# Kernel optimization log

Hardware: AMD Instinct MI355X
Metric: run time of the kernel (lower is better)

## Reference

```python
import jax, jax.numpy as jnp
import numpy as np

B, D, H, O, E = 16384, 256, 256, 256, 32
N_ACTIVE = 22          # int(32 * 0.7) from BoltzmannGate
TEMP = float(np.e)     # Boltzmann temperature
EPS = 1e-8


def setup_inputs() -> dict:
    key = jax.random.key(0)
    ks = jax.random.split(key, 7)
    s = 0.02  # init scale for weights
    return {
        "x":  jax.random.normal(ks[0], (B, D), dtype=jnp.float32),
        "W1": jax.random.normal(ks[1], (E, H, D), dtype=jnp.float32) * s,  # [E, out=H, in=D] torch Linear layout
        "b1": jax.random.normal(ks[2], (E, H), dtype=jnp.float32) * s,
        "W2": jax.random.normal(ks[3], (E, O, H), dtype=jnp.float32) * s,
        "b2": jax.random.normal(ks[4], (E, O), dtype=jnp.float32) * s,
        "Wg": jax.random.normal(ks[5], (E, D), dtype=jnp.float32) * s,
        "bg": jax.random.normal(ks[6], (E,), dtype=jnp.float32) * s,
    }


def reference(x, W1, b1, W2, b2, Wg, bg):
    # Dense all-experts forward: [B, E, H] -> relu -> [B, E, O]
    h = jax.nn.relu(jnp.einsum('bd,ehd->beh', x, W1) + b1[None, :, :])
    expert_out = jnp.einsum('beh,eoh->beo', h, W2) + b2[None, :, :]

    # Boltzmann gate: softmax(scores / T), keep top-k probs, renormalize.
    scores = (x @ Wg.T + bg) / TEMP                      # [B, E]
    probs = jax.nn.softmax(scores, axis=-1)
    _, topk_idx = jax.lax.top_k(probs, N_ACTIVE)         # [B, N_ACTIVE]
    mask = jnp.zeros_like(probs).at[jnp.arange(B)[:, None], topk_idx].set(1.0)
    weights = probs * mask
    weights = weights / (jnp.sum(weights, axis=-1, keepdims=True) + EPS)

    # Weighted combine over experts: [B, O]
    return jnp.einsum('be,beo->bo', weights, expert_out)
```

## Files before the change

kernel.cpp:

```cpp
#include <hip/hip_runtime.h>
#include <hip/hip_bf16.h>


typedef __attribute__((ext_vector_type(8))) short bf16x8;
typedef __attribute__((ext_vector_type(4))) float f32x4;

__device__ __forceinline__ unsigned short f2bf(float f) {
    unsigned u = __builtin_bit_cast(unsigned, f);
    u += 0x7FFFu + ((u >> 16) & 1u);
    return (unsigned short)(u >> 16);
}
__device__ __forceinline__ unsigned pack_bf16x2(float a, float b) {
    return (unsigned)f2bf(a) | ((unsigned)f2bf(b) << 16);
}

#define LX(r, ch) (((r) << 8) + ((((ch) ^ ((r) & 7))) << 3))

__global__ __launch_bounds__(256) void cvt_w(const float* __restrict__ W1,
                                             const float* __restrict__ W2,
                                             unsigned short* __restrict__ Wr) {
    int T = blockIdx.x * 256 + threadIdx.x;
    int lane = T & 63, t = (T >> 6) & 3, kb = (T >> 8) & 7;
    int g = (T >> 11) & 7, e = T >> 14;
    int l15 = lane & 15, quad = lane >> 4;
    int row = (g & 3) * 64 + t * 16 + l15;
    const float* src = ((g < 4) ? W1 : W2) +
                       ((long)e * 256 + row) * 256 + kb * 32 + quad * 8;
    float4 v0 = ((const float4*)src)[0], v1 = ((const float4*)src)[1];
    uint4 o;
    o.x = pack_bf16x2(v0.x, v0.y); o.y = pack_bf16x2(v0.z, v0.w);
    o.z = pack_bf16x2(v1.x, v1.y); o.w = pack_bf16x2(v1.z, v1.w);
    ((uint4*)Wr)[T] = o;
}

__global__ __launch_bounds__(512, 2) void moe_kernel(
    const float* __restrict__ x,
    const unsigned short* __restrict__ Wr,
    const float* __restrict__ bias1,
    const float* __restrict__ b2,
    const float* __restrict__ Wg,
    const float* __restrict__ bg,
    float* __restrict__ out)
{
    __shared__ __align__(16) unsigned short x_s[64 * 256];
    __shared__ __align__(16) unsigned short h_s[64 * 256];
    __shared__ float gws[64 * 33];

    const int tid  = threadIdx.x;
    const int wv   = tid >> 6, lane = tid & 63;
    const int quad = lane >> 4, l15 = lane & 15;
    const int crew = wv >> 2, g = wv & 3;
    const int row0 = blockIdx.x * 64;

#pragma unroll
    for (int c = 0; c < 4; ++c) {
        int chunk = tid + c * 512;
        int r = chunk >> 5, ch = chunk & 31;
        const float4* s = (const float4*)(x + (long)(row0 + r) * 256 + ch * 8);
        float4 v0 = s[0], v1 = s[1];
        uint4 o;
        o.x = pack_bf16x2(v0.x, v0.y); o.y = pack_bf16x2(v0.z, v0.w);
        o.z = pack_bf16x2(v1.x, v1.y); o.w = pack_bf16x2(v1.z, v1.w);
        *(uint4*)(&x_s[LX(r, ch)]) = o;
    }

    {
        const int e32 = lane & 31, half = lane >> 5;
        const float4* wg4 = (const float4*)(Wg + e32 * 256 + half * 128);
        float bgv = bg[e32];
        for (int i = 0; i < 8; ++i) {
            int lr = wv * 8 + i;
            const float4* xr4 = (const float4*)(x + (long)(row0 + lr) * 256 + half * 128);
            float acc = 0.f;
#pragma unroll
            for (int tt = 0; tt < 32; ++tt) {
                float4 w = wg4[tt], xv = xr4[tt];
                acc = fmaf(w.x, xv.x, acc); acc = fmaf(w.y, xv.y, acc);
                acc = fmaf(w.z, xv.z, acc); acc = fmaf(w.w, xv.w, acc);
            }
            acc += __shfl_xor(acc, 32);
            float score = (acc + bgv) / 2.71828182845904523f;

            float m = score;
#pragma unroll
            for (int d = 16; d >= 1; d >>= 1) m = fmaxf(m, __shfl_xor(m, d));
            float p = expf(score - m);
            float ps = p;
#pragma unroll
            for (int d = 16; d >= 1; d >>= 1) ps += __shfl_xor(ps, d);
            float prob = p / ps;

            int rank = 0;
#pragma unroll
            for (int j = 0; j < 32; ++j) {
                float pj = __shfl(prob, j);
                rank += (pj > prob || (pj == prob && j < e32)) ? 1 : 0;
            }
            float kept = (rank < 22) ? prob : 0.f;
            float wsum = kept;
#pragma unroll
            for (int d = 16; d >= 1; d >>= 1) wsum += __shfl_xor(wsum, d);
            float weight = kept / (wsum + 1e-8f);

            if (half == 0) gws[lr * 33 + e32] = weight;
        }
    }

    __syncthreads();

    f32x4 oacc[4][4];
#pragma unroll
    for (int ot = 0; ot < 4; ++ot)
#pragma unroll
        for (int rt = 0; rt < 4; ++rt) {
            f32x4 z = {0.f, 0.f, 0.f, 0.f};
            oacc[ot][rt] = z;
        }
    if (crew == 1) {
        for (int ee = 0; ee < 32; ++ee) {
            float gv[4];
#pragma unroll
            for (int rt = 0; rt < 4; ++rt) gv[rt] = gws[(rt * 16 + l15) * 33 + ee];
#pragma unroll
            for (int ot = 0; ot < 4; ++ot) {
                float4 bb = *(const float4*)(b2 + ee * 256 + g * 64 + ot * 16 + quad * 4);
#pragma unroll
                for (int rt = 0; rt < 4; ++rt) {
                    oacc[ot][rt][0] = fmaf(gv[rt], bb.x, oacc[ot][rt][0]);
                    oacc[ot][rt][1] = fmaf(gv[rt], bb.y, oacc[ot][rt][1]);
                    oacc[ot][rt][2] = fmaf(gv[rt], bb.z, oacc[ot][rt][2]);
                    oacc[ot][rt][3] = fmaf(gv[rt], bb.w, oacc[ot][rt][3]);
                }
            }
        }
    }

    bf16x8 buf[4];
    {
        const unsigned short* p0 = Wr + ((long)wv * 8) * 2048;
#pragma unroll
        for (int t = 0; t < 4; ++t)
            buf[t] = *(const bf16x8*)(p0 + t * 512 + lane * 8);
    }

    for (int e = 0; e <= 32; ++e) {
        f32x4 hacc[4][4];
        if (crew == 0) {
            if (e < 32) {
#pragma unroll
                for (int ht = 0; ht < 4; ++ht)
#pragma unroll
                    for (int rt = 0; rt < 4; ++rt) {
                        f32x4 z = {0.f, 0.f, 0.f, 0.f};
                        hacc[ht][rt] = z;
                    }
                const unsigned short* wcur = Wr + ((long)(e * 8 + wv) * 8) * 2048;
                const unsigned short* wnxt = Wr + ((long)((e + 1) * 8 + wv) * 8) * 2048;
#pragma unroll
                for (int kb = 0; kb < 8; ++kb) {
                    bf16x8 a[4];
#pragma unroll
                    for (int t = 0; t < 4; ++t) a[t] = buf[t];
                    const unsigned short* np = (kb < 7) ? (wcur + (kb + 1) * 2048) : wnxt;
#pragma unroll
                    for (int t = 0; t < 4; ++t)
                        buf[t] = *(const bf16x8*)(np + t * 512 + lane * 8);
                    bf16x8 bb[4];
#pragma unroll
                    for (int rt = 0; rt < 4; ++rt)
                        bb[rt] = *(const bf16x8*)(&x_s[LX(rt * 16 + l15, kb * 4 + quad)]);
#pragma unroll
                    for (int ht = 0; ht < 4; ++ht)
#pragma unroll
                        for (int rt = 0; rt < 4; ++rt)
                            hacc[ht][rt] = __builtin_amdgcn_mfma_f32_16x16x32_bf16(
                                a[ht], bb[rt], hacc[ht][rt], 0, 0, 0);
                }
            }
        } else {
            if (e >= 1) {
                const int me = e - 1;
                const unsigned short* wcur = Wr + ((long)(me * 8 + wv) * 8) * 2048;
                const unsigned short* wnxt = Wr + ((long)((me + 1) * 8 + wv) * 8) * 2048;
#pragma unroll
                for (int kb = 0; kb < 8; ++kb) {
                    bf16x8 a[4];
#pragma unroll
                    for (int t = 0; t < 4; ++t) a[t] = buf[t];
                    const unsigned short* np = (kb < 7) ? (wcur + (kb + 1) * 2048) : wnxt;
#pragma unroll
                    for (int t = 0; t < 4; ++t)
                        buf[t] = *(const bf16x8*)(np + t * 512 + lane * 8);
                    bf16x8 bb[4];
#pragma unroll
                    for (int rt = 0; rt < 4; ++rt)
                        bb[rt] = *(const bf16x8*)(&h_s[LX(rt * 16 + l15, kb * 4 + quad)]);
#pragma unroll
                    for (int ot = 0; ot < 4; ++ot)
#pragma unroll
                        for (int rt = 0; rt < 4; ++rt)
                            oacc[ot][rt] = __builtin_amdgcn_mfma_f32_16x16x32_bf16(
                                a[ot], bb[rt], oacc[ot][rt], 0, 0, 0);
                }
            }
        }

        __syncthreads();

        if (crew == 0 && e < 32) {
            float4 bv[4]; float gw[4];
#pragma unroll
            for (int ht = 0; ht < 4; ++ht)
                bv[ht] = *(const float4*)(bias1 + e * 256 + g * 64 + ht * 16 + quad * 4);
#pragma unroll
            for (int rt = 0; rt < 4; ++rt)
                gw[rt] = gws[(rt * 16 + l15) * 33 + e];
#pragma unroll
            for (int ht = 0; ht < 4; ++ht) {
                int hb = g * 64 + ht * 16 + quad * 4;
                int ch = hb >> 3, off = hb & 7;
#pragma unroll
                for (int rt = 0; rt < 4; ++rt) {
                    int r = rt * 16 + l15;
                    float v0 = fmaxf(hacc[ht][rt][0] + bv[ht].x, 0.f) * gw[rt];
                    float v1 = fmaxf(hacc[ht][rt][1] + bv[ht].y, 0.f) * gw[rt];
                    float v2 = fmaxf(hacc[ht][rt][2] + bv[ht].z, 0.f) * gw[rt];
                    float v3 = fmaxf(hacc[ht][rt][3] + bv[ht].w, 0.f) * gw[rt];
                    uint2 p;
                    p.x = pack_bf16x2(v0, v1);
                    p.y = pack_bf16x2(v2, v3);
                    *(uint2*)(&h_s[(r << 8) + ((ch ^ (r & 7)) << 3) + off]) = p;
                }
            }
        }

        __syncthreads();
    }

    if (crew == 1) {
#pragma unroll
        for (int ot = 0; ot < 4; ++ot)
#pragma unroll
            for (int rt = 0; rt < 4; ++rt)
                *(f32x4*)(out + (long)(row0 + rt * 16 + l15) * 256 +
                          g * 64 + ot * 16 + quad * 4) = oacc[ot][rt];
    }
}

extern "C" void kernel_launch(void* const* d_in, const int* in_sizes, int n_in,
                              void* d_out, int out_size, void* d_ws, size_t ws_size,
                              hipStream_t stream) {
    (void)in_sizes; (void)n_in; (void)out_size; (void)ws_size;
    const float* x  = (const float*)d_in[0];
    const float* W1 = (const float*)d_in[1];
    const float* b1 = (const float*)d_in[2];
    const float* W2 = (const float*)d_in[3];
    const float* b2 = (const float*)d_in[4];
    const float* Wg = (const float*)d_in[5];
    const float* bg = (const float*)d_in[6];
    float* out = (float*)d_out;

    unsigned short* Wr = (unsigned short*)d_ws;

    cvt_w<<<2048, 256, 0, stream>>>(W1, W2, Wr);
    moe_kernel<<<256, 512, 0, stream>>>(x, Wr, b1, b2, Wg, bg, out);
}
```

Baseline: 312.3 us.

## Split experts across two blocks with 128-row tiles and combine partial outputs

Each block now handles 128 rows and half of the experts (16), so every weight fragment loaded from global memory feeds twice as many MFMAs. The two expert halves write separate partial outputs, which a new combine kernel sums. Weight prefetch is deepened to two k-steps, and barriers become a raw lgkmcnt wait plus s_barrier. In exchange, LDS use doubles to about 136 KB, which likely drops residency to one block per CU, accumulator registers double, and the partial output adds an extra global round-trip through a workspace buffer.

```diff
diff --git a/kernel.cpp b/kernel.cpp
--- a/kernel.cpp
+++ b/kernel.cpp
@@ -12,6 +12,10 @@
 }
 __device__ __forceinline__ unsigned pack_bf16x2(float a, float b) {
     return (unsigned)f2bf(a) | ((unsigned)f2bf(b) << 16);
+}
+
+__device__ __forceinline__ void lds_barrier() {
+    asm volatile("s_waitcnt lgkmcnt(0)\n\ts_barrier" ::: "memory");
 }
 
 #define LX(r, ch) (((r) << 8) + ((((ch) ^ ((r) & 7))) << 3))
@@ -40,20 +44,24 @@
     const float* __restrict__ b2,
     const float* __restrict__ Wg,
     const float* __restrict__ bg,
-    float* __restrict__ out)
+    float* __restrict__ out,
+    float* __restrict__ part1)
 {
-    __shared__ __align__(16) unsigned short x_s[64 * 256];
-    __shared__ __align__(16) unsigned short h_s[64 * 256];
-    __shared__ float gws[64 * 33];
+    __shared__ __align__(16) unsigned short x_s[128 * 256];
+    __shared__ __align__(16) unsigned short h_s[128 * 256];
+    __shared__ float gws[128 * 17];
 
     const int tid  = threadIdx.x;
     const int wv   = tid >> 6, lane = tid & 63;
     const int quad = lane >> 4, l15 = lane & 15;
     const int crew = wv >> 2, g = wv & 3;
-    const int row0 = blockIdx.x * 64;
-
-#pragma unroll
-    for (int c = 0; c < 4; ++c) {
+    const int eg   = blockIdx.x & 1;
+    const int rg   = blockIdx.x >> 1;
+    const int row0 = rg * 128;
+    const int ebase = eg * 16;
+
+#pragma unroll
+    for (int c = 0; c < 8; ++c) {
         int chunk = tid + c * 512;
         int r = chunk >> 5, ch = chunk & 31;
         const float4* s = (const float4*)(x + (long)(row0 + r) * 256 + ch * 8);
@@ -68,8 +76,8 @@
         const int e32 = lane & 31, half = lane >> 5;
         const float4* wg4 = (const float4*)(Wg + e32 * 256 + half * 128);
         float bgv = bg[e32];
-        for (int i = 0; i < 8; ++i) {
-            int lr = wv * 8 + i;
+        for (int i = 0; i < 16; ++i) {
+            int lr = wv * 16 + i;
             const float4* xr4 = (const float4*)(x + (long)(row0 + lr) * 256 + half * 128);
             float acc = 0.f;
 #pragma unroll
@@ -102,30 +110,31 @@
             for (int d = 16; d >= 1; d >>= 1) wsum += __shfl_xor(wsum, d);
             float weight = kept / (wsum + 1e-8f);
 
-            if (half == 0) gws[lr * 33 + e32] = weight;
-        }
-    }
-
-    __syncthreads();
-
-    f32x4 oacc[4][4];
+            if (half == 0 && (e32 >> 4) == eg)
+                gws[lr * 17 + (e32 & 15)] = weight;
+        }
+    }
+
+    lds_barrier();
+
+    f32x4 oacc[4][8];
 #pragma unroll
     for (int ot = 0; ot < 4; ++ot)
 #pragma unroll
-        for (int rt = 0; rt < 4; ++rt) {
+        for (int rt = 0; rt < 8; ++rt) {
             f32x4 z = {0.f, 0.f, 0.f, 0.f};
             oacc[ot][rt] = z;
         }
     if (crew == 1) {
-        for (int ee = 0; ee < 32; ++ee) {
-            float gv[4];
-#pragma unroll
-            for (int rt = 0; rt < 4; ++rt) gv[rt] = gws[(rt * 16 + l15) * 33 + ee];
+        for (int ee = 0; ee < 16; ++ee) {
+            float gv[8];
+#pragma unroll
+            for (int rt = 0; rt < 8; ++rt) gv[rt] = gws[(rt * 16 + l15) * 17 + ee];
 #pragma unroll
             for (int ot = 0; ot < 4; ++ot) {
-                float4 bb = *(const float4*)(b2 + ee * 256 + g * 64 + ot * 16 + quad * 4);
-#pragma unroll
-                for (int rt = 0; rt < 4; ++rt) {
+                float4 bb = *(const float4*)(b2 + (ebase + ee) * 256 + g * 64 + ot * 16 + quad * 4);
+#pragma unroll
+                for (int rt = 0; rt < 8; ++rt) {
                     oacc[ot][rt][0] = fmaf(gv[rt], bb.x, oacc[ot][rt][0]);
                     oacc[ot][rt][1] = fmaf(gv[rt], bb.y, oacc[ot][rt][1]);
                     oacc[ot][rt][2] = fmaf(gv[rt], bb.z, oacc[ot][rt][2]);
@@ -135,92 +144,92 @@
         }
     }
 
-    bf16x8 buf[4];
-    {
-        const unsigned short* p0 = Wr + ((long)wv * 8) * 2048;
-#pragma unroll
-        for (int t = 0; t < 4; ++t)
-            buf[t] = *(const bf16x8*)(p0 + t * 512 + lane * 8);
-    }
-
-    for (int e = 0; e <= 32; ++e) {
-        f32x4 hacc[4][4];
+    const unsigned short* wbase = Wr + ((long)ebase * 8 + wv) * 16384;
+
+    bf16x8 q0[4], q1[4];
+#pragma unroll
+    for (int t = 0; t < 4; ++t) q0[t] = *(const bf16x8*)(wbase + t * 512 + lane * 8);
+#pragma unroll
+    for (int t = 0; t < 4; ++t) q1[t] = *(const bf16x8*)(wbase + 2048 + t * 512 + lane * 8);
+
+#pragma unroll 1
+    for (int e = 0; e <= 16; ++e) {
+        f32x4 hacc[4][8];
         if (crew == 0) {
-            if (e < 32) {
+            if (e < 16) {
 #pragma unroll
                 for (int ht = 0; ht < 4; ++ht)
 #pragma unroll
-                    for (int rt = 0; rt < 4; ++rt) {
+                    for (int rt = 0; rt < 8; ++rt) {
                         f32x4 z = {0.f, 0.f, 0.f, 0.f};
                         hacc[ht][rt] = z;
                     }
-                const unsigned short* wcur = Wr + ((long)(e * 8 + wv) * 8) * 2048;
-                const unsigned short* wnxt = Wr + ((long)((e + 1) * 8 + wv) * 8) * 2048;
+                const unsigned short* wcur = wbase + (long)e * 131072;
 #pragma unroll
                 for (int kb = 0; kb < 8; ++kb) {
-                    bf16x8 a[4];
-#pragma unroll
-                    for (int t = 0; t < 4; ++t) a[t] = buf[t];
-                    const unsigned short* np = (kb < 7) ? (wcur + (kb + 1) * 2048) : wnxt;
+                    bf16x8 bx[8];
+#pragma unroll
+                    for (int rt = 0; rt < 8; ++rt)
+                        bx[rt] = *(const bf16x8*)(&x_s[LX(rt * 16 + l15, kb * 4 + quad)]);
+#pragma unroll
+                    for (int ht = 0; ht < 4; ++ht)
+#pragma unroll
+                        for (int rt = 0; rt < 8; ++rt)
+                            hacc[ht][rt] = __builtin_amdgcn_mfma_f32_16x16x32_bf16(
+                                q0[ht], bx[rt], hacc[ht][rt], 0, 0, 0);
+#pragma unroll
+                    for (int t = 0; t < 4; ++t) q0[t] = q1[t];
+                    const unsigned short* pf = (kb < 6)
+                        ? (wcur + (kb + 2) * 2048)
+                        : (wcur + 131072 + (kb - 6) * 2048);
 #pragma unroll
                     for (int t = 0; t < 4; ++t)
-                        buf[t] = *(const bf16x8*)(np + t * 512 + lane * 8);
-                    bf16x8 bb[4];
-#pragma unroll
-                    for (int rt = 0; rt < 4; ++rt)
-                        bb[rt] = *(const bf16x8*)(&x_s[LX(rt * 16 + l15, kb * 4 + quad)]);
-#pragma unroll
-                    for (int ht = 0; ht < 4; ++ht)
-#pragma unroll
-                        for (int rt = 0; rt < 4; ++rt)
-                            hacc[ht][rt] = __builtin_amdgcn_mfma_f32_16x16x32_bf16(
-                                a[ht], bb[rt], hacc[ht][rt], 0, 0, 0);
+                        q1[t] = *(const bf16x8*)(pf + t * 512 + lane * 8);
                 }
             }
         } else {
             if (e >= 1) {
-                const int me = e - 1;
-                const unsigned short* wcur = Wr + ((long)(me * 8 + wv) * 8) * 2048;
-                const unsigned short* wnxt = Wr + ((long)((me + 1) * 8 + wv) * 8) * 2048;
+                const unsigned short* wcur = wbase + (long)(e - 1) * 131072;
 #pragma unroll
                 for (int kb = 0; kb < 8; ++kb) {
-                    bf16x8 a[4];
-#pragma unroll
-                    for (int t = 0; t < 4; ++t) a[t] = buf[t];
-                    const unsigned short* np = (kb < 7) ? (wcur + (kb + 1) * 2048) : wnxt;
+                    bf16x8 bx[8];
+#pragma unroll
+                    for (int rt = 0; rt < 8; ++rt)
+                        bx[rt] = *(const bf16x8*)(&h_s[LX(rt * 16 + l15, kb * 4 + quad)]);
+#pragma unroll
+                    for (int ot = 0; ot < 4; ++ot)
+#pragma unroll
+                        for (int rt = 0; rt < 8; ++rt)
+                            oacc[ot][rt] = __builtin_amdgcn_mfma_f32_16x16x32_bf16(
+                                q0[ot], bx[rt], oacc[ot][rt], 0, 0, 0);
+#pragma unroll
+                    for (int t = 0; t < 4; ++t) q0[t] = q1[t];
+                    const unsigned short* pf = (kb < 6)
+                        ? (wcur + (kb + 2) * 2048)
+                        : (wcur + 131072 + (kb - 6) * 2048);
 #pragma unroll
                     for (int t = 0; t < 4; ++t)
-                        buf[t] = *(const bf16x8*)(np + t * 512 + lane * 8);
-                    bf16x8 bb[4];
-#pragma unroll
-                    for (int rt = 0; rt < 4; ++rt)
-                        bb[rt] = *(const bf16x8*)(&h_s[LX(rt * 16 + l15, kb * 4 + quad)]);
-#pragma unroll
-                    for (int ot = 0; ot < 4; ++ot)
-#pragma unroll
-                        for (int rt = 0; rt < 4; ++rt)
-                            oacc[ot][rt] = __builtin_amdgcn_mfma_f32_16x16x32_bf16(
-                                a[ot], bb[rt], oacc[ot][rt], 0, 0, 0);
-                }
-            }
-        }
-
-        __syncthreads();
-
-        if (crew == 0 && e < 32) {
-            float4 bv[4]; float gw[4];
+                        q1[t] = *(const bf16x8*)(pf + t * 512 + lane * 8);
+                }
+            }
+        }
+
+        lds_barrier();
+
+        if (crew == 0 && e < 16) {
+            float4 bv[4]; float gw[8];
 #pragma unroll
             for (int ht = 0; ht < 4; ++ht)
-                bv[ht] = *(const float4*)(bias1 + e * 256 + g * 64 + ht * 16 + quad * 4);
-#pragma unroll
-            for (int rt = 0; rt < 4; ++rt)
-                gw[rt] = gws[(rt * 16 + l15) * 33 + e];
+                bv[ht] = *(const float4*)(bias1 + (ebase + e) * 256 + g * 64 + ht * 16 + quad * 4);
+#pragma unroll
+            for (int rt = 0; rt < 8; ++rt)
+                gw[rt] = gws[(rt * 16 + l15) * 17 + e];
 #pragma unroll
             for (int ht = 0; ht < 4; ++ht) {
                 int hb = g * 64 + ht * 16 + quad * 4;
                 int ch = hb >> 3, off = hb & 7;
 #pragma unroll
-                for (int rt = 0; rt < 4; ++rt) {
+                for (int rt = 0; rt < 8; ++rt) {
                     int r = rt * 16 + l15;
                     float v0 = fmaxf(hacc[ht][rt][0] + bv[ht].x, 0.f) * gw[rt];
                     float v1 = fmaxf(hacc[ht][rt][1] + bv[ht].y, 0.f) * gw[rt];
@@ -234,17 +243,27 @@
             }
         }
 
-        __syncthreads();
+        lds_barrier();
     }
 
     if (crew == 1) {
+        float* po = ((eg == 0) ? out : part1) + (long)row0 * 256;
 #pragma unroll
         for (int ot = 0; ot < 4; ++ot)
 #pragma unroll
-            for (int rt = 0; rt < 4; ++rt)
-                *(f32x4*)(out + (long)(row0 + rt * 16 + l15) * 256 +
+            for (int rt = 0; rt < 8; ++rt)
+                *(f32x4*)(po + (long)(rt * 16 + l15) * 256 +
                           g * 64 + ot * 16 + quad * 4) = oacc[ot][rt];
     }
+}
+
+__global__ __launch_bounds__(256) void combine(const float* __restrict__ p1,
+                                               float* __restrict__ out) {
+    int i = blockIdx.x * 256 + threadIdx.x;
+    float4 a = ((const float4*)out)[i];
+    float4 b = ((const float4*)p1)[i];
+    a.x += b.x; a.y += b.y; a.z += b.z; a.w += b.w;
+    ((float4*)out)[i] = a;
 }
 
 extern "C" void kernel_launch(void* const* d_in, const int* in_sizes, int n_in,
@@ -260,8 +279,10 @@
     const float* bg = (const float*)d_in[6];
     float* out = (float*)d_out;
 
-    unsigned short* Wr = (unsigned short*)d_ws;
+    unsigned short* Wr    = (unsigned short*)d_ws;
+    float*          part1 = (float*)((char*)d_ws + (16u << 20));
 
     cvt_w<<<2048, 256, 0, stream>>>(W1, W2, Wr);
-    moe_kernel<<<256, 512, 0, stream>>>(x, Wr, b1, b2, Wg, bg, out);
-}
+    moe_kernel<<<256, 512, 0, stream>>>(x, Wr, b1, b2, Wg, bg, out, part1);
+    combine<<<4096, 256, 0, stream>>>(part1, out);
+}
```

New measurement: 603.7 us. +93.3%, slower.
